# Kernel tuning notes

Hardware: AMD Instinct MI355X
Metric: run time of the kernel (lower is better)

## Reference

```python
import jax, jax.numpy as jnp
import numpy as np

K = 3        # attention kernel size
PAD = 1      # padding
C = 20       # out_channels (hidden_dim_1)
HALF = C // 2
POOL = 4     # MaxPool2d((1, 4))
OUT_DIM = 80


def setup_inputs() -> dict:
    key = jax.random.key(0)
    ks = jax.random.split(key, 8)
    T, D = 1024, 1280
    lin_in = C * D // POOL  # 6400
    return {
        "feature": jax.random.normal(ks[0], (T, D), jnp.float32),
        "wq": jax.random.normal(ks[1], (C, 1), jnp.float32),
        "wk": jax.random.normal(ks[2], (C, 1), jnp.float32),
        "wv": jax.random.normal(ks[3], (C, 1), jnp.float32),
        "rel_h": jax.random.normal(ks[4], (HALF, K), jnp.float32),
        "rel_w": jax.random.normal(ks[5], (HALF, K), jnp.float32),
        "dense_w": jax.random.normal(ks[6], (OUT_DIM, lin_in), jnp.float32) * 0.02,
        "dense_b": jax.random.normal(ks[7], (OUT_DIM,), jnp.float32) * 0.02,
    }


def reference(feature, wq, wk, wv, rel_h, rel_w, dense_w, dense_b):
    T, D = feature.shape
    W = D // POOL
    # MaxPool2d((1, POOL)) over last dim of [1,1,T,D]
    x = feature.reshape(T, W, POOL).max(axis=-1)[None, None]  # [1,1,T,W]

    # 1x1 convs (in_channels=1) are just channel outer products
    q = jnp.einsum('bihw,oi->bohw', x, wq)                    # [1,C,T,W]
    xp = jnp.pad(x, ((0, 0), (0, 0), (PAD, PAD), (PAD, PAD)))
    k = jnp.einsum('bihw,oi->bohw', xp, wk)                   # [1,C,T+2,W+2]
    v = jnp.einsum('bihw,oi->bohw', xp, wv)

    # unfold(2,K,1).unfold(3,K,1) -> windows flattened as (i_h*K + i_w)
    def windows(t):
        return jnp.stack([t[:, :, i:i + T, j:j + W]
                          for i in range(K) for j in range(K)], axis=-1)  # [1,C,T,W,K*K]

    k_win = windows(k)
    v_win = windows(v)

    # relative positional bias: first HALF channels get rel_h (varies along h),
    # second HALF get rel_w (varies along w); flattened to K*K in (h,w) order
    rel = jnp.concatenate([
        jnp.broadcast_to(rel_h[:, :, None], (HALF, K, K)),
        jnp.broadcast_to(rel_w[:, None, :], (HALF, K, K)),
    ], axis=0).reshape(C, K * K)
    k_win = k_win + rel[None, :, None, None, :]

    attn = jax.nn.softmax(q[..., None] * k_win, axis=-1)      # [1,C,T,W,9]
    out = jnp.sum(attn * v_win, axis=-1)                      # [1,C,T,W]
    out = jax.nn.relu(out)

    # torch: transpose(0,1) -> [C,1,T,W] then view(-1, C*W): channel-major flatten
    flat = out[0].reshape(-1, C * W)                          # [T, C*W]
    y = flat @ dense_w.T + dense_b                            # [T, OUT_DIM]
    # torch: stack -> [T,1,OUT], transpose(0,1) -> [1,T,OUT]
    return y[None, :, :]
```

## Files before the change

### kernel.cpp

```cpp
#include <hip/hip_runtime.h>
#include <hip/hip_bf16.h>

#define TT   1024
#define DD   1280
#define WW   320
#define CC   20
#define HALF 10
#define TW   (TT*WW)
#define LIN  (CC*WW)
#define OUTD 80
#define NSPLIT 20
#define LOG2E 1.4426950408889634f
#define XPAD 384

#define POOL_BLOCKS (TW/256)
#define CVT_BLOCKS  ((OUTD*LIN)/(256*8))

typedef __attribute__((ext_vector_type(4))) float f32x4;
typedef __attribute__((ext_vector_type(8))) short bf16x8;

__device__ __forceinline__ ushort f2bf(float v) {
    unsigned u = __float_as_uint(v);
    u += 0x7FFFu + ((u >> 16) & 1u);
    return (ushort)(u >> 16);
}

__device__ __forceinline__ unsigned pk_bf16(float lo, float hi) {
    unsigned r;
    asm("v_cvt_pk_bf16_f32 %0, %1, %2" : "=v"(r) : "v"(lo), "v"(hi));
    return r;
}

__global__ __launch_bounds__(256) void k_prep(const float* __restrict__ f,
                                              float* __restrict__ x,
                                              const float* __restrict__ dw,
                                              ushort* __restrict__ dwb) {
    int b = blockIdx.x;
    if (b < POOL_BLOCKS) {
        int idx = b * 256 + threadIdx.x;
        float4 v = reinterpret_cast<const float4*>(f)[idx];
        x[idx] = fmaxf(fmaxf(v.x, v.y), fmaxf(v.z, v.w));
    } else {
        int i = ((b - POOL_BLOCKS) * 256 + threadIdx.x) * 8;
        float4 a = reinterpret_cast<const float4*>(dw + i)[0];
        float4 c = reinterpret_cast<const float4*>(dw + i)[1];
        reinterpret_cast<ushort4*>(dwb + i)[0] =
            make_ushort4(f2bf(a.x), f2bf(a.y), f2bf(a.z), f2bf(a.w));
        reinterpret_cast<ushort4*>(dwb + i)[1] =
            make_ushort4(f2bf(c.x), f2bf(c.y), f2bf(c.z), f2bf(c.w));
    }
}

__global__ __launch_bounds__(256, 5) void k_fused(const float* __restrict__ x,
                                                  const float* __restrict__ wq,
                                                  const float* __restrict__ wk,
                                                  const float* __restrict__ wv,
                                                  const float* __restrict__ rh,
                                                  const float* __restrict__ rw,
                                                  const ushort* __restrict__ dwb,
                                                  float* __restrict__ part) {
    __shared__ __align__(16) ushort alds[16][328];
    __shared__ float red[16][81];

    int tid = threadIdx.x;
    int mt  = blockIdx.x;
    int sp  = blockIdx.y;

    {
        int j  = tid >> 4;
        int wg = tid & 15;
        int ct = (mt * 16 + j) * 20 + sp;
        int t  = ct & 1023;
        int c  = ct >> 10;
        bool ish = (c < HALF);

        float wqc = wq[c];
        float qk  = wqc * wk[c] * LOG2E;
        float vv  = wv[c];
        const float* rp = ish ? (rh + c * 3) : (rw + (c - HALF) * 3);
        float r0 = wqc * rp[0] * LOG2E;
        float r1 = wqc * rp[1] * LOG2E;
        float r2 = wqc * rp[2] * LOG2E;
        float Bco[9];
        #pragma unroll
        for (int i = 0; i < 9; ++i) {
            float bh = (i < 3) ? r0 : ((i < 6) ? r1 : r2);
            float bw = ((i % 3) == 0) ? r0 : (((i % 3) == 1) ? r1 : r2);
            Bco[i] = ish ? bh : bw;
        }

        bool rok0 = (t > 0), rok2 = (t < TT - 1);
        const float* xb0 = x + t * WW;

        for (int u = 0; u < 5; ++u) {
            int gg = wg + 16 * u;
            int w0 = gg * 4;
            float xr[3][6];
            #pragma unroll
            for (int dt = 0; dt < 3; ++dt) {
                const float* rpx = xb0 + (dt - 1) * WW + w0;
                float4 va = *reinterpret_cast<const float4*>(rpx - 4);
                float4 vb = *reinterpret_cast<const float4*>(rpx);
                float  vc = rpx[4];
                bool rok = (dt == 1) ? true : ((dt == 0) ? rok0 : rok2);
                xr[dt][0] = (rok & (gg > 0))  ? va.w : 0.f;
                xr[dt][1] = rok ? vb.x : 0.f;
                xr[dt][2] = rok ? vb.y : 0.f;
                xr[dt][3] = rok ? vb.z : 0.f;
                xr[dt][4] = rok ? vb.w : 0.f;
                xr[dt][5] = (rok & (gg < 79)) ? vc : 0.f;
            }

            float o[4];
            #pragma unroll
            for (int p = 0; p < 4; ++p) {
                float xc = xr[1][p + 1];
                float a  = qk * xc;
                float s[9];
                #pragma unroll
                for (int i = 0; i < 9; ++i)
                    s[i] = fmaf(a, xr[i / 3][p + i % 3], Bco[i] * xc);
                float m012 = fmaxf(fmaxf(s[0], s[1]), s[2]);
                float m345 = fmaxf(fmaxf(s[3], s[4]), s[5]);
                float m678 = fmaxf(fmaxf(s[6], s[7]), s[8]);
                float m    = fmaxf(fmaxf(m012, m345), m678);
                float den0 = 0.f, den1 = 0.f, num0 = 0.f, num1 = 0.f;
                #pragma unroll
                for (int i = 0; i < 9; ++i) {
                    float e = __builtin_amdgcn_exp2f(s[i] - m);
                    if (i & 1) { den1 += e; num1 = fmaf(e, xr[i / 3][p + i % 3], num1); }
                    else       { den0 += e; num0 = fmaf(e, xr[i / 3][p + i % 3], num0); }
                }
                float den = den0 + den1, num = num0 + num1;
                o[p] = fmaxf(vv * (num * __builtin_amdgcn_rcpf(den)), 0.0f);
            }
            *reinterpret_cast<uint2*>(&alds[j][w0]) =
                make_uint2(pk_bf16(o[0], o[1]), pk_bf16(o[2], o[3]));
        }
    }

    __syncthreads();

    int wave = tid >> 6;
    int lane = tid & 63;
    int r16  = lane & 15;
    int kg   = lane >> 4;

    int ks0 = (wave < 2) ? wave * 3 : 6 + (wave - 2) * 2;
    int ksn = (wave < 2) ? 3 : 2;

    const ushort* bp = dwb + (size_t)r16 * LIN + sp * 320 + kg * 8;

    f32x4 acc[5] = {};
    for (int ks = ks0; ks < ks0 + ksn; ++ks) {
        bf16x8 af = *reinterpret_cast<const bf16x8*>(&alds[r16][ks * 32 + kg * 8]);
        #pragma unroll
        for (int jj = 0; jj < 5; ++jj) {
            bf16x8 bfr = *reinterpret_cast<const bf16x8*>(bp + ks * 32 + (size_t)jj * 16 * LIN);
            acc[jj] = __builtin_amdgcn_mfma_f32_16x16x32_bf16(af, bfr, acc[jj], 0, 0, 0);
        }
    }

    for (int v = 0; v < 4; ++v) {
        __syncthreads();
        if (wave == v) {
            #pragma unroll
            for (int jj = 0; jj < 5; ++jj)
                #pragma unroll
                for (int r = 0; r < 4; ++r) {
                    int row = kg * 4 + r, col = jj * 16 + r16;
                    if (v == 0) red[row][col]  = acc[jj][r];
                    else        red[row][col] += acc[jj][r];
                }
        }
    }
    __syncthreads();

    float* pp = part + (size_t)sp * TT * OUTD + (size_t)(mt * 16) * OUTD;
    for (int i2 = tid; i2 < 16 * 80; i2 += 256)
        pp[i2] = red[i2 / 80][i2 % 80];
}

__global__ __launch_bounds__(256) void k_reduce(const float* __restrict__ part,
                                                const float* __restrict__ bias,
                                                float* __restrict__ out) {
    int idx = blockIdx.x * 256 + threadIdx.x;
    int o = idx % OUTD;
    float s = bias[o];
    #pragma unroll
    for (int sp = 0; sp < NSPLIT; ++sp) s += part[(size_t)sp * TT * OUTD + idx];
    out[idx] = s;
}

extern "C" void kernel_launch(void* const* d_in, const int* in_sizes, int n_in,
                              void* d_out, int out_size, void* d_ws, size_t ws_size,
                              hipStream_t stream) {
    const float* feature = (const float*)d_in[0];
    const float* wq      = (const float*)d_in[1];
    const float* wk      = (const float*)d_in[2];
    const float* wv      = (const float*)d_in[3];
    const float* rel_h   = (const float*)d_in[4];
    const float* rel_w   = (const float*)d_in[5];
    const float* dense_w = (const float*)d_in[6];
    const float* dense_b = (const float*)d_in[7];
    float* out = (float*)d_out;

    float*  ws   = (float*)d_ws;
    float*  x    = ws + XPAD;
    ushort* dwb  = (ushort*)(ws + 2 * XPAD + TW);
    float*  part = (float*)(dwb + (size_t)OUTD * LIN);

    k_prep  <<<POOL_BLOCKS + CVT_BLOCKS, 256, 0, stream>>>(feature, x, dense_w, dwb);
    k_fused <<<dim3(TT/16, NSPLIT), 256, 0, stream>>>(x, wq, wk, wv, rel_h, rel_w, dwb, part);
    k_reduce<<<(TT*OUTD)/256, 256, 0, stream>>>(part, dense_b, out);
}
```

Measured before the change: 33.11 us.

## Specialize attention math per channel half, parallelize LDS reduction, vectorize reduce kernel

The attention score computation gets a template specialization per channel half, so the relative bias is folded into precomputed per-row terms (G) and fewer multiplies are needed per score. The serialized four-step cross-wave reduction with its barriers is replaced by separate per-wave LDS slices that are summed at write-out, which quadruples the reduction shared memory. The split-K reduce kernel now processes four outputs per thread using float4 loads, cutting its launch to a quarter of the blocks. The larger LDS footprint may reduce occupancy, and the branch between specializations is uniform per thread but not necessarily per wave.

```diff
diff --git a/kernel.cpp b/kernel.cpp
--- a/kernel.cpp
+++ b/kernel.cpp
@@ -51,6 +51,49 @@
     }
 }
 
+template<bool ISH>
+__device__ __forceinline__ uint2 attn_group(const float xr[3][6], float qk,
+                                            float r0, float r1, float r2, float vv) {
+    float G[3][6];
+    #pragma unroll
+    for (int dt = 0; dt < 3; ++dt) {
+        float rdt = (dt == 0) ? r0 : ((dt == 1) ? r1 : r2);
+        #pragma unroll
+        for (int idx = 0; idx < 6; ++idx)
+            G[dt][idx] = ISH ? fmaf(qk, xr[dt][idx], rdt) : (qk * xr[dt][idx]);
+    }
+    float o[4];
+    #pragma unroll
+    for (int p = 0; p < 4; ++p) {
+        float xc = xr[1][p + 1];
+        float s[9];
+        if (ISH) {
+            #pragma unroll
+            for (int i = 0; i < 9; ++i) s[i] = xc * G[i / 3][p + i % 3];
+        } else {
+            float bb0 = r0 * xc, bb1 = r1 * xc, bb2 = r2 * xc;
+            #pragma unroll
+            for (int i = 0; i < 9; ++i) {
+                float bbw = ((i % 3) == 0) ? bb0 : (((i % 3) == 1) ? bb1 : bb2);
+                s[i] = fmaf(xc, G[i / 3][p + i % 3], bbw);
+            }
+        }
+        float m = fmaxf(fmaxf(fmaxf(fmaxf(s[0], s[1]), s[2]),
+                              fmaxf(fmaxf(s[3], s[4]), s[5])),
+                        fmaxf(fmaxf(s[6], s[7]), s[8]));
+        float den0 = 0.f, den1 = 0.f, num0 = 0.f, num1 = 0.f;
+        #pragma unroll
+        for (int i = 0; i < 9; ++i) {
+            float e = __builtin_amdgcn_exp2f(s[i] - m);
+            if (i & 1) { den1 += e; num1 = fmaf(e, xr[i / 3][p + i % 3], num1); }
+            else       { den0 += e; num0 = fmaf(e, xr[i / 3][p + i % 3], num0); }
+        }
+        float den = den0 + den1, num = num0 + num1;
+        o[p] = fmaxf(vv * (num * __builtin_amdgcn_rcpf(den)), 0.0f);
+    }
+    return make_uint2(pk_bf16(o[0], o[1]), pk_bf16(o[2], o[3]));
+}
+
 __global__ __launch_bounds__(256, 5) void k_fused(const float* __restrict__ x,
                                                   const float* __restrict__ wq,
                                                   const float* __restrict__ wk,
@@ -60,7 +103,7 @@
                                                   const ushort* __restrict__ dwb,
                                                   float* __restrict__ part) {
     __shared__ __align__(16) ushort alds[16][328];
-    __shared__ float red[16][81];
+    __shared__ float red[4][16][81];
 
     int tid = threadIdx.x;
     int mt  = blockIdx.x;
@@ -81,13 +124,6 @@
         float r0 = wqc * rp[0] * LOG2E;
         float r1 = wqc * rp[1] * LOG2E;
         float r2 = wqc * rp[2] * LOG2E;
-        float Bco[9];
-        #pragma unroll
-        for (int i = 0; i < 9; ++i) {
-            float bh = (i < 3) ? r0 : ((i < 6) ? r1 : r2);
-            float bw = ((i % 3) == 0) ? r0 : (((i % 3) == 1) ? r1 : r2);
-            Bco[i] = ish ? bh : bw;
-        }
 
         bool rok0 = (t > 0), rok2 = (t < TT - 1);
         const float* xb0 = x + t * WW;
@@ -110,32 +146,9 @@
                 xr[dt][4] = rok ? vb.w : 0.f;
                 xr[dt][5] = (rok & (gg < 79)) ? vc : 0.f;
             }
-
-            float o[4];
-            #pragma unroll
-            for (int p = 0; p < 4; ++p) {
-                float xc = xr[1][p + 1];
-                float a  = qk * xc;
-                float s[9];
-                #pragma unroll
-                for (int i = 0; i < 9; ++i)
-                    s[i] = fmaf(a, xr[i / 3][p + i % 3], Bco[i] * xc);
-                float m012 = fmaxf(fmaxf(s[0], s[1]), s[2]);
-                float m345 = fmaxf(fmaxf(s[3], s[4]), s[5]);
-                float m678 = fmaxf(fmaxf(s[6], s[7]), s[8]);
-                float m    = fmaxf(fmaxf(m012, m345), m678);
-                float den0 = 0.f, den1 = 0.f, num0 = 0.f, num1 = 0.f;
-                #pragma unroll
-                for (int i = 0; i < 9; ++i) {
-                    float e = __builtin_amdgcn_exp2f(s[i] - m);
-                    if (i & 1) { den1 += e; num1 = fmaf(e, xr[i / 3][p + i % 3], num1); }
-                    else       { den0 += e; num0 = fmaf(e, xr[i / 3][p + i % 3], num0); }
-                }
-                float den = den0 + den1, num = num0 + num1;
-                o[p] = fmaxf(vv * (num * __builtin_amdgcn_rcpf(den)), 0.0f);
-            }
-            *reinterpret_cast<uint2*>(&alds[j][w0]) =
-                make_uint2(pk_bf16(o[0], o[1]), pk_bf16(o[2], o[3]));
+            uint2 res = ish ? attn_group<true >(xr, qk, r0, r1, r2, vv)
+                            : attn_group<false>(xr, qk, r0, r1, r2, vv);
+            *reinterpret_cast<uint2*>(&alds[j][w0]) = res;
         }
     }
 
@@ -161,35 +174,34 @@
         }
     }
 
-    for (int v = 0; v < 4; ++v) {
-        __syncthreads();
-        if (wave == v) {
-            #pragma unroll
-            for (int jj = 0; jj < 5; ++jj)
-                #pragma unroll
-                for (int r = 0; r < 4; ++r) {
-                    int row = kg * 4 + r, col = jj * 16 + r16;
-                    if (v == 0) red[row][col]  = acc[jj][r];
-                    else        red[row][col] += acc[jj][r];
-                }
-        }
-    }
+    #pragma unroll
+    for (int jj = 0; jj < 5; ++jj)
+        #pragma unroll
+        for (int r = 0; r < 4; ++r)
+            red[wave][kg * 4 + r][jj * 16 + r16] = acc[jj][r];
     __syncthreads();
 
     float* pp = part + (size_t)sp * TT * OUTD + (size_t)(mt * 16) * OUTD;
-    for (int i2 = tid; i2 < 16 * 80; i2 += 256)
-        pp[i2] = red[i2 / 80][i2 % 80];
+    #pragma unroll
+    for (int i2 = tid; i2 < 16 * 80; i2 += 256) {
+        int row = i2 / 80, col = i2 % 80;
+        pp[i2] = (red[0][row][col] + red[1][row][col]) +
+                 (red[2][row][col] + red[3][row][col]);
+    }
 }
 
 __global__ __launch_bounds__(256) void k_reduce(const float* __restrict__ part,
                                                 const float* __restrict__ bias,
                                                 float* __restrict__ out) {
-    int idx = blockIdx.x * 256 + threadIdx.x;
-    int o = idx % OUTD;
-    float s = bias[o];
-    #pragma unroll
-    for (int sp = 0; sp < NSPLIT; ++sp) s += part[(size_t)sp * TT * OUTD + idx];
-    out[idx] = s;
+    int idx4 = (blockIdx.x * 256 + threadIdx.x) * 4;
+    int o = idx4 % OUTD;
+    float4 s = *reinterpret_cast<const float4*>(bias + o);
+    #pragma unroll
+    for (int sp = 0; sp < NSPLIT; ++sp) {
+        float4 p = *reinterpret_cast<const float4*>(part + (size_t)sp * TT * OUTD + idx4);
+        s.x += p.x; s.y += p.y; s.z += p.z; s.w += p.w;
+    }
+    *reinterpret_cast<float4*>(out + idx4) = s;
 }
 
 extern "C" void kernel_launch(void* const* d_in, const int* in_sizes, int n_in,
@@ -212,5 +224,5 @@
 
     k_prep  <<<POOL_BLOCKS + CVT_BLOCKS, 256, 0, stream>>>(feature, x, dense_w, dwb);
     k_fused <<<dim3(TT/16, NSPLIT), 256, 0, stream>>>(x, wq, wk, wv, rel_h, rel_w, dwb, part);
-    k_reduce<<<(TT*OUTD)/256, 256, 0, stream>>>(part, dense_b, out);
-}
+    k_reduce<<<(TT*OUTD)/(256*4), 256, 0, stream>>>(part, dense_b, out);
+}
```

Result: no change. 33.14 us (+0.1%).
